# Optimization experiments

Hardware: AMD Instinct MI355X
Metric: run time of the kernel (lower is better)

The kernel has to match this reference:

```python
import jax, jax.numpy as jnp
import numpy as np
import math

B, N, M, H, DV, DE, KV, KE = 2, 4096, 12288, 8, 256, 256, 16, 16
DK = DV // H
LN_EPS = 1e-5


def _split_heads(x, h):
    b, n, d = x.shape
    return x.reshape(b, n, h, d // h).transpose(0, 2, 1, 3)  # (b,h,n,dk)


def _layernorm(x):
    # LayerNorm(elementwise_affine=False) over last dim, applied per head
    mu = jnp.mean(x, axis=-1, keepdims=True)
    var = jnp.mean(jnp.square(x - mu), axis=-1, keepdims=True)
    return (x - mu) * jax.lax.rsqrt(var + LN_EPS)


def _sparse_attention(x, q, k, idx):
    # x,q,k: (b,h,N,dk); idx: (N,kk) local neighborhoods
    dk = q.shape[-1]
    k_g = k[:, :, idx, :]  # (b,h,N,kk,dk)
    x_g = x[:, :, idx, :]  # (b,h,N,kk,dk)
    scores = jnp.einsum('bhnd,bhnkd->bhnk', q, k_g) / math.sqrt(dk)
    attn = jax.nn.softmax(scores, axis=-1)
    return jnp.einsum('bhnk,bhnkd->bhnd', attn, x_g)


def setup_inputs() -> dict:
    key = jax.random.key(0)
    ks = jax.random.split(key, 10)
    scale = 1.0 / math.sqrt(DV)
    return {
        'x_v': jax.random.normal(ks[0], (B, N, DV), jnp.float32),
        'x_e': jax.random.normal(ks[1], (B, M, DE), jnp.float32),
        'd_0': jax.random.normal(ks[2], (B, M, N), jnp.float32),
        'W_vQ': jax.random.normal(ks[3], (DV, DV), jnp.float32) * scale,
        'W_vK': jax.random.normal(ks[4], (DV, DV), jnp.float32) * scale,
        'W_vV': jax.random.normal(ks[5], (DV, DV), jnp.float32) * scale,
        'W_eQ': jax.random.normal(ks[6], (DE, DE), jnp.float32) * scale,
        'W_eK': jax.random.normal(ks[7], (DE, DE), jnp.float32) * scale,
        'v_idx': jax.random.randint(ks[8], (N, KV), 0, N, jnp.int32),
        'e_idx': jax.random.randint(ks[9], (M, KE), 0, M, jnp.int32),
    }


def reference(x_v, x_e, d_0, W_vQ, W_vK, W_vV, W_eQ, W_eK, v_idx, e_idx):
    # Q/K/V projections (nn.Linear, bias=False): y = x @ W.T
    v_Q = _layernorm(_split_heads(jnp.einsum('bnd,ed->bne', x_v, W_vQ), H))
    v_K = _layernorm(_split_heads(jnp.einsum('bnd,ed->bne', x_v, W_vK), H))
    v_V = _split_heads(jnp.einsum('bnd,ed->bne', x_v, W_vV), H)
    e_Q = _layernorm(_split_heads(jnp.einsum('bmd,ed->bme', x_e, W_eQ), H))
    e_K = _layernorm(_split_heads(jnp.einsum('bmd,ed->bme', x_e, W_eK), H))

    # d_0 @ v_V per head (boundary op: vertices -> edges)
    x = jnp.einsum('bmn,bhnd->bhmd', d_0, v_V)
    # grouped Hodge op on edges (inv=False -> q=e_Q, k=e_K)
    x = _sparse_attention(x, e_Q, e_K, e_idx)
    # d_0.T @ x per head (edges -> vertices)
    x = jnp.einsum('bmn,bhmd->bhnd', d_0, x)
    # grouped Hodge op on vertices (inv=True swaps -> q=v_K, k=v_Q)
    x = _sparse_attention(x, v_K, v_Q, v_idx)

    # merge heads -> (b, n, d_v)
    return x.transpose(0, 2, 1, 3).reshape(B, N, DV)
```

## Files before the change

### kernel.cpp

```cpp
#include <hip/hip_runtime.h>

#define BB 2
#define NN 4096
#define MM 12288
#define HH 8
#define CC 256

typedef float f32x4 __attribute__((ext_vector_type(4)));
typedef __bf16 bf16x8 __attribute__((ext_vector_type(8)));

__device__ __forceinline__ unsigned short f2bf(float f) {
    union { float f; unsigned u; } v; v.f = f;
    unsigned r = (v.u + 0x7FFFu + ((v.u >> 16) & 1u)) >> 16;
    return (unsigned short)r;
}
__device__ __forceinline__ unsigned pk2(float a, float b) {
    return (unsigned)f2bf(a) | ((unsigned)f2bf(b) << 16);
}
__device__ __forceinline__ void gll16(const unsigned short* g, unsigned short* l) {
    __builtin_amdgcn_global_load_lds(
        (__attribute__((address_space(1))) void*)(g),
        (__attribute__((address_space(3))) void*)(l), 16, 0, 0);
}

__global__ __launch_bounds__(256) void proj_kernel(
    const float* __restrict__ X, const float* __restrict__ W,
    float* __restrict__ outF, unsigned short* __restrict__ outT,
    int Nb, int mode)
{
    __shared__ unsigned short Al[64][264];
    __shared__ unsigned short Wl[32][264];
    const int t = threadIdx.x;
    const long rowbase = (long)blockIdx.x * 64;
    const int lane = t & 63, w = t >> 6, q = lane >> 4, l15 = lane & 15;

    {
        const float* Xp = X + rowbase * CC;
        #pragma unroll
        for (int i = 0; i < 16; ++i) {
            int f = t + i * 256;
            int row = f >> 6, k4 = (f & 63) << 2;
            f32x4 v = *(const f32x4*)(Xp + row * CC + k4);
            *(uint2*)(&Al[row][k4]) = make_uint2(pk2(v[0], v[1]), pk2(v[2], v[3]));
        }
    }

    const int wrow = w * 16;
    for (int ct = 0; ct < 8; ++ct) {
        __syncthreads();
        #pragma unroll
        for (int i = 0; i < 8; ++i) {
            int f = t + i * 256;
            int row = f >> 6, k4 = (f & 63) << 2;
            f32x4 v = *(const f32x4*)(W + (ct * 32 + row) * CC + k4);
            *(uint2*)(&Wl[row][k4]) = make_uint2(pk2(v[0], v[1]), pk2(v[2], v[3]));
        }
        __syncthreads();
        f32x4 acc0 = {0.f, 0.f, 0.f, 0.f}, acc1 = {0.f, 0.f, 0.f, 0.f};
        #pragma unroll
        for (int kk = 0; kk < 8; ++kk) {
            bf16x8 af = *(const bf16x8*)(&Al[wrow + l15][kk * 32 + q * 8]);
            bf16x8 b0 = *(const bf16x8*)(&Wl[l15][kk * 32 + q * 8]);
            bf16x8 b1 = *(const bf16x8*)(&Wl[16 + l15][kk * 32 + q * 8]);
            acc0 = __builtin_amdgcn_mfma_f32_16x16x32_bf16(af, b0, acc0, 0, 0, 0);
            acc1 = __builtin_amdgcn_mfma_f32_16x16x32_bf16(af, b1, acc1, 0, 0, 0);
        }
        if (mode == 0) {
            #pragma unroll
            for (int r = 0; r < 4; ++r) {
                float s = acc0[r] + acc1[r];
                s += __shfl_xor(s, 1); s += __shfl_xor(s, 2);
                s += __shfl_xor(s, 4); s += __shfl_xor(s, 8);
                float mu = s * (1.0f / 32.0f);
                float a0 = acc0[r] - mu, a1 = acc1[r] - mu;
                float sq = a0 * a0 + a1 * a1;
                sq += __shfl_xor(sq, 1); sq += __shfl_xor(sq, 2);
                sq += __shfl_xor(sq, 4); sq += __shfl_xor(sq, 8);
                float rs = rsqrtf(sq * (1.0f / 32.0f) + 1e-5f);
                long row = rowbase + wrow + q * 4 + r;
                outF[row * CC + ct * 32 + l15] = a0 * rs;
                outF[row * CC + ct * 32 + 16 + l15] = a1 * rs;
            }
        } else {
            long row = rowbase + wrow + q * 4;
            int b = (row >= Nb) ? 1 : 0;
            long n = row - (long)b * Nb;
            int c0 = ct * 32 + l15;
            unsigned short* p0 = outT + ((long)(b * CC + c0)) * Nb + n;
            *(uint2*)p0 = make_uint2(pk2(acc0[0], acc0[1]), pk2(acc0[2], acc0[3]));
            unsigned short* p1 = outT + ((long)(b * CC + c0 + 16)) * Nb + n;
            *(uint2*)p1 = make_uint2(pk2(acc1[0], acc1[1]), pk2(acc1[2], acc1[3]));
        }
    }
}

__global__ __launch_bounds__(256) void attnw_kernel(
    const float* __restrict__ Q, const float* __restrict__ K,
    const int* __restrict__ idx, float* __restrict__ wout, int R)
{
    long tid = (long)blockIdx.x * 256 + threadIdx.x;
    int h = (int)(tid & 7);
    long br = tid >> 3;
    int b = (br >= R) ? 1 : 0;
    long r = br - (long)b * R;
    const float* qp = Q + br * CC + h * 32;
    f32x4 qv[8];
    #pragma unroll
    for (int i = 0; i < 8; ++i) qv[i] = *(const f32x4*)(qp + 4 * i);
    const int* ip = idx + r * 16;
    float sc[16];
    #pragma unroll
    for (int k = 0; k < 16; ++k) {
        const float* kp = K + ((long)b * R + ip[k]) * CC + h * 32;
        float d = 0.f;
        #pragma unroll
        for (int i = 0; i < 8; ++i) {
            f32x4 kv = *(const f32x4*)(kp + 4 * i);
            d += qv[i][0] * kv[0] + qv[i][1] * kv[1] + qv[i][2] * kv[2] + qv[i][3] * kv[3];
        }
        sc[k] = d * 0.17677669529663687f;
    }
    float mx = sc[0];
    #pragma unroll
    for (int k = 1; k < 16; ++k) mx = fmaxf(mx, sc[k]);
    float sum = 0.f;
    #pragma unroll
    for (int k = 0; k < 16; ++k) { sc[k] = __expf(sc[k] - mx); sum += sc[k]; }
    float inv = 1.0f / sum;
    float* op = wout + tid * 16;
    #pragma unroll
    for (int i = 0; i < 4; ++i) {
        f32x4 v = { sc[4*i] * inv, sc[4*i+1] * inv, sc[4*i+2] * inv, sc[4*i+3] * inv };
        *(f32x4*)(op + 4 * i) = v;
    }
}

__global__ __launch_bounds__(256) void cvt_kernel(
    const float* __restrict__ d0, unsigned short* __restrict__ d0b,
    unsigned short* __restrict__ d0t)
{
    __shared__ unsigned short T[64][66];
    const int t = threadIdx.x;
    const int b = blockIdx.z;
    const long n0 = (long)blockIdx.x * 64;
    const long m0 = (long)blockIdx.y * 64;
    const int r = t >> 4, c4 = (t & 15) << 2;
    const float* src = d0 + ((long)b * MM + m0) * NN + n0;
    #pragma unroll
    for (int i = 0; i < 4; ++i) {
        int row = r + i * 16;
        f32x4 v = *(const f32x4*)(src + (long)row * NN + c4);
        *(uint2*)(d0b + ((long)b * MM + m0 + row) * NN + n0 + c4) =
            make_uint2(pk2(v[0], v[1]), pk2(v[2], v[3]));
        T[row][c4 + 0] = f2bf(v[0]);
        T[row][c4 + 1] = f2bf(v[1]);
        T[row][c4 + 2] = f2bf(v[2]);
        T[row][c4 + 3] = f2bf(v[3]);
    }
    __syncthreads();
    #pragma unroll
    for (int i = 0; i < 4; ++i) {
        int rn = r + i * 16;
        unsigned lo = (unsigned)T[c4 + 0][rn] | ((unsigned)T[c4 + 1][rn] << 16);
        unsigned hi = (unsigned)T[c4 + 2][rn] | ((unsigned)T[c4 + 3][rn] << 16);
        *(uint2*)(d0t + ((long)b * NN + n0 + rn) * MM + m0 + c4) = make_uint2(lo, hi);
    }
}

template<int RB, int NSPLIT, int LD>
__global__ __launch_bounds__(256) void gemm_kernel(
    const unsigned short* __restrict__ A, const unsigned short* __restrict__ Bm,
    float* __restrict__ out)
{
    constexpr int KS = LD / NSPLIT;
    __shared__ unsigned short Al[128 * 64];
    __shared__ unsigned short Bl[128 * 64];
    const int t = threadIdx.x;
    const int b = blockIdx.z / NSPLIT, s = blockIdx.z % NSPLIT;
    const long m0 = (long)blockIdx.x * 128;
    const int c0 = blockIdx.y * 128;
    const int w = t >> 6, lane = t & 63;
    const int q = lane >> 4, l15 = lane & 15;
    const int wr = (w >> 1) * 64, wc = (w & 1) * 64;
    const unsigned short* Ab = A + ((long)b * RB + m0) * LD + (long)s * KS;
    const unsigned short* Bb = Bm + ((long)b * CC + c0) * LD + (long)s * KS;
    const long laneOff = (long)(lane >> 3) * LD + (lane & 7) * 8;

    f32x4 acc[4][4];
    #pragma unroll
    for (int i = 0; i < 4; ++i)
        #pragma unroll
        for (int j = 0; j < 4; ++j) acc[i][j] = {0.f, 0.f, 0.f, 0.f};

    for (int k0 = 0; k0 < KS; k0 += 64) {
        #pragma unroll
        for (int j = 0; j < 4; ++j) {
            const int ch = w + 4 * j;
            gll16(Ab + (long)(ch * 8) * LD + k0 + laneOff, Al + ch * 512);
            gll16(Bb + (long)(ch * 8) * LD + k0 + laneOff, Bl + ch * 512);
        }
        __syncthreads();
        #pragma unroll
        for (int kh = 0; kh < 2; ++kh) {
            bf16x8 af[4], bfr[4];
            #pragma unroll
            for (int i = 0; i < 4; ++i)
                af[i] = *(const bf16x8*)(Al + (wr + i * 16 + l15) * 64 + kh * 32 + q * 8);
            #pragma unroll
            for (int j = 0; j < 4; ++j)
                bfr[j] = *(const bf16x8*)(Bl + (wc + j * 16 + l15) * 64 + kh * 32 + q * 8);
            #pragma unroll
            for (int i = 0; i < 4; ++i)
                #pragma unroll
                for (int j = 0; j < 4; ++j)
                    acc[i][j] = __builtin_amdgcn_mfma_f32_16x16x32_bf16(af[i], bfr[j], acc[i][j], 0, 0, 0);
        }
        __syncthreads();
    }

    float* ob = out + (((long)s * BB + b) * RB + m0) * CC + c0;
    #pragma unroll
    for (int i = 0; i < 4; ++i)
        #pragma unroll
        for (int j = 0; j < 4; ++j)
            #pragma unroll
            for (int r = 0; r < 4; ++r)
                ob[(long)(wr + i * 16 + q * 4 + r) * CC + wc + j * 16 + l15] = acc[i][j][r];
}

__global__ __launch_bounds__(256) void gather_e_kernel(
    const float* __restrict__ x1, const float* __restrict__ ae,
    const int* __restrict__ eidx, unsigned short* __restrict__ x2t)
{
    __shared__ unsigned short T[256][72];
    const int t = threadIdx.x;
    const int b = blockIdx.y;
    const int m0 = blockIdx.x * 64;
    const int h = t >> 5;
    const float* xa = x1 + (long)b * MM * CC;
    const float* xb = x1 + ((long)BB + b) * MM * CC;
    for (int ml = 0; ml < 64; ++ml) {
        int m = m0 + ml;
        const int* ip = eidx + (long)m * 16;
        const float* wp = ae + ((long)b * MM + m) * 128 + h * 16;
        float acc = 0.f;
        #pragma unroll
        for (int k = 0; k < 16; ++k) {
            long o = (long)ip[k] * CC + t;
            acc += wp[k] * (xa[o] + xb[o]);
        }
        T[t][ml] = f2bf(acc);
    }
    __syncthreads();
    unsigned short* dst = x2t + ((long)b * CC + t) * MM + m0;
    #pragma unroll
    for (int i = 0; i < 8; ++i)
        *(uint4*)(dst + i * 8) = *(const uint4*)(&T[t][i * 8]);
}

__global__ __launch_bounds__(256) void gather_v_kernel(
    const float* __restrict__ x3, const float* __restrict__ av,
    const int* __restrict__ vidx, float* __restrict__ out)
{
    const int t = threadIdx.x;
    const int b = blockIdx.y;
    const int n = blockIdx.x;
    const int h = t >> 5;
    const float* x0 = x3 + ((long)(0 * BB + b)) * NN * CC;
    const float* x1p = x3 + ((long)(1 * BB + b)) * NN * CC;
    const float* x2p = x3 + ((long)(2 * BB + b)) * NN * CC;
    const float* x3p = x3 + ((long)(3 * BB + b)) * NN * CC;
    const int* ip = vidx + (long)n * 16;
    const float* wp = av + ((long)b * NN + n) * 128 + h * 16;
    float acc = 0.f;
    #pragma unroll
    for (int k = 0; k < 16; ++k) {
        long j = (long)ip[k] * CC + t;
        acc += wp[k] * (x0[j] + x1p[j] + x2p[j] + x3p[j]);
    }
    out[((long)b * NN + n) * CC + t] = acc;
}

extern "C" void kernel_launch(void* const* d_in, const int* in_sizes, int n_in,
                              void* d_out, int out_size, void* d_ws, size_t ws_size,
                              hipStream_t stream)
{
    const float* x_v = (const float*)d_in[0];
    const float* x_e = (const float*)d_in[1];
    const float* d0  = (const float*)d_in[2];
    const float* WvQ = (const float*)d_in[3];
    const float* WvK = (const float*)d_in[4];
    const float* WvV = (const float*)d_in[5];
    const float* WeQ = (const float*)d_in[6];
    const float* WeK = (const float*)d_in[7];
    const int* vidx  = (const int*)d_in[8];
    const int* eidx  = (const int*)d_in[9];

    char* ws = (char*)d_ws;
    const size_t oVVt = 0;
    const size_t oAv  = oVVt + 4194304;
    const size_t oX2t = oAv  + 4194304;
    const size_t oD0t = oX2t + 12582912;
    const size_t oAe  = oD0t + 201326592;
    const size_t oVQ  = oAe  + 12582912;
    const size_t oVK  = oVQ  + 8388608;
    const size_t oR1  = oVK  + 8388608;
    const size_t oR2  = oR1  + 50331648;
    const size_t total = oR2 + 201326592;
    if (total > ws_size) return;

    unsigned short* vVt = (unsigned short*)(ws + oVVt);
    float*          av  = (float*)(ws + oAv);
    unsigned short* x2t = (unsigned short*)(ws + oX2t);
    unsigned short* d0t = (unsigned short*)(ws + oD0t);
    float*          ae  = (float*)(ws + oAe);
    float*          vQ  = (float*)(ws + oVQ);
    float*          vK  = (float*)(ws + oVK);
    float*          eQ  = (float*)(ws + oR1);
    float*          eK  = (float*)(ws + oR1 + 25165824);
    float*          x1  = (float*)(ws + oR1);
    unsigned short* d0b = (unsigned short*)(ws + oR2);
    float*          x3  = (float*)(ws + oR2);

    proj_kernel<<<dim3((BB * NN) / 64), 256, 0, stream>>>(x_v, WvQ, vQ, nullptr, NN, 0);
    proj_kernel<<<dim3((BB * NN) / 64), 256, 0, stream>>>(x_v, WvK, vK, nullptr, NN, 0);
    proj_kernel<<<dim3((BB * NN) / 64), 256, 0, stream>>>(x_v, WvV, nullptr, vVt, NN, 1);
    proj_kernel<<<dim3((BB * MM) / 64), 256, 0, stream>>>(x_e, WeQ, eQ, nullptr, MM, 0);
    proj_kernel<<<dim3((BB * MM) / 64), 256, 0, stream>>>(x_e, WeK, eK, nullptr, MM, 0);
    attnw_kernel<<<dim3((BB * MM * HH) / 256), 256, 0, stream>>>(eQ, eK, eidx, ae, MM);
    attnw_kernel<<<dim3((BB * NN * HH) / 256), 256, 0, stream>>>(vK, vQ, vidx, av, NN);
    cvt_kernel<<<dim3(NN / 64, MM / 64, BB), 256, 0, stream>>>(d0, d0b, d0t);
    gemm_kernel<MM, 2, NN><<<dim3(MM / 128, 2, BB * 2), 256, 0, stream>>>(d0b, vVt, x1);
    gather_e_kernel<<<dim3(MM / 64, BB), 256, 0, stream>>>(x1, ae, eidx, x2t);
    gemm_kernel<NN, 4, MM><<<dim3(NN / 128, 2, BB * 4), 256, 0, stream>>>(d0t, x2t, x3);
    gather_v_kernel<<<dim3(NN, BB), 256, 0, stream>>>(x3, av, vidx, (float*)d_out);
}
```

Before: 1.244 ms.

## Fuse projection launches, prefetch weights, and store split-K partials as bf16

The five projection launches become two templated launches. Each block handles several weight matrices over half of the output columns, and the next weight chunk is prefetched into registers before the MFMA loop. The split-K GEMM partial outputs (x1, x3) are written as bf16 instead of fp32, which halves their write and gather read traffic. The gather_e kernel is also split over two channel halves for more parallelism. The bf16 partials lose precision before the reduction, and the workspace layout is changed so the partial buffers alias the eQ/eK regions.

New measurement: 1.003 ms. 19.4% less time.

```diff
diff --git a/kernel.cpp b/kernel.cpp
--- a/kernel.cpp
+++ b/kernel.cpp
@@ -14,6 +14,9 @@
     unsigned r = (v.u + 0x7FFFu + ((v.u >> 16) & 1u)) >> 16;
     return (unsigned short)r;
 }
+__device__ __forceinline__ float bf2f(unsigned short u) {
+    union { unsigned u; float f; } v; v.u = ((unsigned)u) << 16; return v.f;
+}
 __device__ __forceinline__ unsigned pk2(float a, float b) {
     return (unsigned)f2bf(a) | ((unsigned)f2bf(b) << 16);
 }
@@ -23,15 +26,18 @@
         (__attribute__((address_space(3))) void*)(l), 16, 0, 0);
 }
 
+template<int NW>
 __global__ __launch_bounds__(256) void proj_kernel(
-    const float* __restrict__ X, const float* __restrict__ W,
-    float* __restrict__ outF, unsigned short* __restrict__ outT,
-    int Nb, int mode)
+    const float* __restrict__ X, const float* __restrict__ W0,
+    const float* __restrict__ W1, const float* __restrict__ W2,
+    float* __restrict__ outQ, float* __restrict__ outK,
+    unsigned short* __restrict__ outT, int Nb)
 {
     __shared__ unsigned short Al[64][264];
     __shared__ unsigned short Wl[32][264];
     const int t = threadIdx.x;
     const long rowbase = (long)blockIdx.x * 64;
+    const int cty = blockIdx.y;
     const int lane = t & 63, w = t >> 6, q = lane >> 4, l15 = lane & 15;
 
     {
@@ -45,17 +51,31 @@
         }
     }
 
-    const int wrow = w * 16;
-    for (int ct = 0; ct < 8; ++ct) {
-        __syncthreads();
+    f32x4 pf[8];
+    auto loadchunk = [&](int g) {
+        const float* Wp = (g >> 2) == 0 ? W0 : ((g >> 2) == 1 ? W1 : W2);
+        int rb = (cty * 4 + (g & 3)) * 32;
         #pragma unroll
         for (int i = 0; i < 8; ++i) {
             int f = t + i * 256;
             int row = f >> 6, k4 = (f & 63) << 2;
-            f32x4 v = *(const f32x4*)(W + (ct * 32 + row) * CC + k4);
-            *(uint2*)(&Wl[row][k4]) = make_uint2(pk2(v[0], v[1]), pk2(v[2], v[3]));
+            pf[i] = *(const f32x4*)(Wp + (rb + row) * CC + k4);
+        }
+    };
+    loadchunk(0);
+
+    const int wrow = w * 16;
+    for (int g = 0; g < NW * 4; ++g) {
+        const int widx = g >> 2;
+        const int ct = cty * 4 + (g & 3);
+        #pragma unroll
+        for (int i = 0; i < 8; ++i) {
+            int f = t + i * 256;
+            int row = f >> 6, k4 = (f & 63) << 2;
+            *(uint2*)(&Wl[row][k4]) = make_uint2(pk2(pf[i][0], pf[i][1]), pk2(pf[i][2], pf[i][3]));
         }
         __syncthreads();
+        if (g + 1 < NW * 4) loadchunk(g + 1);
         f32x4 acc0 = {0.f, 0.f, 0.f, 0.f}, acc1 = {0.f, 0.f, 0.f, 0.f};
         #pragma unroll
         for (int kk = 0; kk < 8; ++kk) {
@@ -65,7 +85,8 @@
             acc0 = __builtin_amdgcn_mfma_f32_16x16x32_bf16(af, b0, acc0, 0, 0, 0);
             acc1 = __builtin_amdgcn_mfma_f32_16x16x32_bf16(af, b1, acc1, 0, 0, 0);
         }
-        if (mode == 0) {
+        if (widx < 2 || NW == 2) {
+            float* outF = (widx == 0) ? outQ : outK;
             #pragma unroll
             for (int r = 0; r < 4; ++r) {
                 float s = acc0[r] + acc1[r];
@@ -91,6 +112,7 @@
             unsigned short* p1 = outT + ((long)(b * CC + c0 + 16)) * Nb + n;
             *(uint2*)p1 = make_uint2(pk2(acc1[0], acc1[1]), pk2(acc1[2], acc1[3]));
         }
+        __syncthreads();
     }
 }
 
@@ -170,7 +192,7 @@
 template<int RB, int NSPLIT, int LD>
 __global__ __launch_bounds__(256) void gemm_kernel(
     const unsigned short* __restrict__ A, const unsigned short* __restrict__ Bm,
-    float* __restrict__ out)
+    unsigned short* __restrict__ out)
 {
     constexpr int KS = LD / NSPLIT;
     __shared__ unsigned short Al[128 * 64];
@@ -218,65 +240,73 @@
         __syncthreads();
     }
 
-    float* ob = out + (((long)s * BB + b) * RB + m0) * CC + c0;
+    unsigned short* ob = out + (((long)s * BB + b) * RB + m0) * CC + c0;
     #pragma unroll
     for (int i = 0; i < 4; ++i)
         #pragma unroll
         for (int j = 0; j < 4; ++j)
             #pragma unroll
             for (int r = 0; r < 4; ++r)
-                ob[(long)(wr + i * 16 + q * 4 + r) * CC + wc + j * 16 + l15] = acc[i][j][r];
+                ob[(long)(wr + i * 16 + q * 4 + r) * CC + wc + j * 16 + l15] = f2bf(acc[i][j][r]);
 }
 
 __global__ __launch_bounds__(256) void gather_e_kernel(
-    const float* __restrict__ x1, const float* __restrict__ ae,
+    const unsigned short* __restrict__ x1, const float* __restrict__ ae,
     const int* __restrict__ eidx, unsigned short* __restrict__ x2t)
 {
-    __shared__ unsigned short T[256][72];
+    __shared__ unsigned short T[128][66];
     const int t = threadIdx.x;
     const int b = blockIdx.y;
     const int m0 = blockIdx.x * 64;
-    const int h = t >> 5;
-    const float* xa = x1 + (long)b * MM * CC;
-    const float* xb = x1 + ((long)BB + b) * MM * CC;
-    for (int ml = 0; ml < 64; ++ml) {
+    const int ch = blockIdx.z;
+    const int cl = t & 127;
+    const int c = ch * 128 + cl;
+    const int mlh = t >> 7;
+    const int h = c >> 5;
+    const unsigned short* xa = x1 + (long)b * MM * CC;
+    const unsigned short* xb = x1 + ((long)BB + b) * MM * CC;
+    for (int mi = 0; mi < 32; ++mi) {
+        int ml = mi * 2 + mlh;
         int m = m0 + ml;
         const int* ip = eidx + (long)m * 16;
         const float* wp = ae + ((long)b * MM + m) * 128 + h * 16;
         float acc = 0.f;
         #pragma unroll
         for (int k = 0; k < 16; ++k) {
-            long o = (long)ip[k] * CC + t;
-            acc += wp[k] * (xa[o] + xb[o]);
-        }
-        T[t][ml] = f2bf(acc);
+            long o = (long)ip[k] * CC + c;
+            acc += wp[k] * (bf2f(xa[o]) + bf2f(xb[o]));
+        }
+        T[cl][ml] = f2bf(acc);
     }
     __syncthreads();
-    unsigned short* dst = x2t + ((long)b * CC + t) * MM + m0;
-    #pragma unroll
-    for (int i = 0; i < 8; ++i)
-        *(uint4*)(dst + i * 8) = *(const uint4*)(&T[t][i * 8]);
+    #pragma unroll
+    for (int i = 0; i < 4; ++i) {
+        int flat = t + i * 256;
+        int rcl = flat >> 3, u4 = flat & 7;
+        unsigned short* dst = x2t + ((long)b * CC + ch * 128 + rcl) * MM + m0 + u4 * 8;
+        *(uint4*)dst = *(const uint4*)(&T[rcl][u4 * 8]);
+    }
 }
 
 __global__ __launch_bounds__(256) void gather_v_kernel(
-    const float* __restrict__ x3, const float* __restrict__ av,
+    const unsigned short* __restrict__ x3, const float* __restrict__ av,
     const int* __restrict__ vidx, float* __restrict__ out)
 {
     const int t = threadIdx.x;
     const int b = blockIdx.y;
     const int n = blockIdx.x;
     const int h = t >> 5;
-    const float* x0 = x3 + ((long)(0 * BB + b)) * NN * CC;
-    const float* x1p = x3 + ((long)(1 * BB + b)) * NN * CC;
-    const float* x2p = x3 + ((long)(2 * BB + b)) * NN * CC;
-    const float* x3p = x3 + ((long)(3 * BB + b)) * NN * CC;
+    const unsigned short* x0 = x3 + ((long)(0 * BB + b)) * NN * CC;
+    const unsigned short* x1p = x3 + ((long)(1 * BB + b)) * NN * CC;
+    const unsigned short* x2p = x3 + ((long)(2 * BB + b)) * NN * CC;
+    const unsigned short* x3p = x3 + ((long)(3 * BB + b)) * NN * CC;
     const int* ip = vidx + (long)n * 16;
     const float* wp = av + ((long)b * NN + n) * 128 + h * 16;
     float acc = 0.f;
     #pragma unroll
     for (int k = 0; k < 16; ++k) {
         long j = (long)ip[k] * CC + t;
-        acc += wp[k] * (x0[j] + x1p[j] + x2p[j] + x3p[j]);
+        acc += wp[k] * (bf2f(x0[j]) + bf2f(x1p[j]) + bf2f(x2p[j]) + bf2f(x3p[j]));
     }
     out[((long)b * NN + n) * CC + t] = acc;
 }
@@ -304,9 +334,10 @@
     const size_t oAe  = oD0t + 201326592;
     const size_t oVQ  = oAe  + 12582912;
     const size_t oVK  = oVQ  + 8388608;
-    const size_t oR1  = oVK  + 8388608;
-    const size_t oR2  = oR1  + 50331648;
-    const size_t total = oR2 + 201326592;
+    const size_t oEQ  = oVK  + 8388608;
+    const size_t oEK  = oEQ  + 25165824;
+    const size_t oD0b = oEK  + 25165824;
+    const size_t total = oD0b + 201326592;
     if (total > ws_size) return;
 
     unsigned short* vVt = (unsigned short*)(ws + oVVt);
@@ -316,22 +347,19 @@
     float*          ae  = (float*)(ws + oAe);
     float*          vQ  = (float*)(ws + oVQ);
     float*          vK  = (float*)(ws + oVK);
-    float*          eQ  = (float*)(ws + oR1);
-    float*          eK  = (float*)(ws + oR1 + 25165824);
-    float*          x1  = (float*)(ws + oR1);
-    unsigned short* d0b = (unsigned short*)(ws + oR2);
-    float*          x3  = (float*)(ws + oR2);
-
-    proj_kernel<<<dim3((BB * NN) / 64), 256, 0, stream>>>(x_v, WvQ, vQ, nullptr, NN, 0);
-    proj_kernel<<<dim3((BB * NN) / 64), 256, 0, stream>>>(x_v, WvK, vK, nullptr, NN, 0);
-    proj_kernel<<<dim3((BB * NN) / 64), 256, 0, stream>>>(x_v, WvV, nullptr, vVt, NN, 1);
-    proj_kernel<<<dim3((BB * MM) / 64), 256, 0, stream>>>(x_e, WeQ, eQ, nullptr, MM, 0);
-    proj_kernel<<<dim3((BB * MM) / 64), 256, 0, stream>>>(x_e, WeK, eK, nullptr, MM, 0);
+    float*          eQ  = (float*)(ws + oEQ);
+    float*          eK  = (float*)(ws + oEK);
+    unsigned short* x1  = (unsigned short*)(ws + oEQ);
+    unsigned short* x3  = (unsigned short*)(ws + oEK);
+    unsigned short* d0b = (unsigned short*)(ws + oD0b);
+
+    proj_kernel<3><<<dim3((BB * NN) / 64, 2), 256, 0, stream>>>(x_v, WvQ, WvK, WvV, vQ, vK, vVt, NN);
+    proj_kernel<2><<<dim3((BB * MM) / 64, 2), 256, 0, stream>>>(x_e, WeQ, WeK, nullptr, eQ, eK, nullptr, MM);
     attnw_kernel<<<dim3((BB * MM * HH) / 256), 256, 0, stream>>>(eQ, eK, eidx, ae, MM);
     attnw_kernel<<<dim3((BB * NN * HH) / 256), 256, 0, stream>>>(vK, vQ, vidx, av, NN);
     cvt_kernel<<<dim3(NN / 64, MM / 64, BB), 256, 0, stream>>>(d0, d0b, d0t);
     gemm_kernel<MM, 2, NN><<<dim3(MM / 128, 2, BB * 2), 256, 0, stream>>>(d0b, vVt, x1);
-    gather_e_kernel<<<dim3(MM / 64, BB), 256, 0, stream>>>(x1, ae, eidx, x2t);
+    gather_e_kernel<<<dim3(MM / 64, BB, 2), 256, 0, stream>>>(x1, ae, eidx, x2t);
     gemm_kernel<NN, 4, MM><<<dim3(NN / 128, 2, BB * 4), 256, 0, stream>>>(d0t, x2t, x3);
     gather_v_kernel<<<dim3(NN, BB), 256, 0, stream>>>(x3, av, vidx, (float*)d_out);
 }
```
